# Kernel optimization log

Hardware: AMD Instinct MI355X
Metric: run time of the kernel (lower is better)

## Reference

```python
import jax, jax.numpy as jnp
import numpy as np
from jax import lax

KERNEL = 3
ALPHA = 0.85
C1 = 0.01 ** 2
C2 = 0.03 ** 2


def _avg_pool(x, k):
    # stride-1 VALID average pool over the last two (H, W) dims of NCHW input
    s = lax.reduce_window(x, 0.0, lax.add, (1, 1, k, k), (1, 1, 1, 1), 'VALID')
    return s / (k * k)


def setup_inputs() -> dict:
    key = jax.random.key(0)
    k1, k2 = jax.random.split(key)
    shape = (4, 3, 1080, 1920)
    pred = jax.random.uniform(k1, shape, dtype=jnp.float32)
    gt = jax.random.uniform(k2, shape, dtype=jnp.float32)
    return {"pred": pred, "gt": gt}


def reference(pred, gt):
    p = (KERNEL - 1) // 2
    # reflection pad H and W
    x = jnp.pad(pred, ((0, 0), (0, 0), (p, p), (p, p)), mode='reflect')
    y = jnp.pad(gt, ((0, 0), (0, 0), (p, p), (p, p)), mode='reflect')

    mu_x = _avg_pool(x, KERNEL)
    mu_y = _avg_pool(y, KERNEL)
    sigma_x = _avg_pool(x * x, KERNEL) - mu_x * mu_x
    sigma_y = _avg_pool(y * y, KERNEL) - mu_y * mu_y
    sigma_xy = _avg_pool(x * y, KERNEL) - mu_x * mu_y

    ssim_n = (2.0 * mu_x * mu_y + C1) * (2.0 * sigma_xy + C2)
    ssim_d = (mu_x * mu_x + mu_y * mu_y + C1) * (sigma_x + sigma_y + C2)
    ssim_pp = jnp.clip((1.0 - ssim_n / ssim_d) * 0.5, 0.0, 1.0)

    ssim_loss = jnp.mean(ssim_pp, axis=1, keepdims=True)   # [B,1,H,W]
    l1_loss = jnp.mean(jnp.abs(pred - gt), axis=1, keepdims=True)
    return ALPHA * ssim_loss + (1.0 - ALPHA) * l1_loss
```

## Files before the change

kernel.cpp:

```cpp
#include <hip/hip_runtime.h>

#define IMG_H 1080
#define IMG_W 1920
#define CH 3

typedef float f32x2 __attribute__((ext_vector_type(2)));

#if __has_builtin(__builtin_elementwise_fma)
#define FMA2(a, b, c) __builtin_elementwise_fma((a), (b), (c))
#else
#define FMA2(a, b, c) ((a) * (b) + (c))
#endif

__global__ __launch_bounds__(256)
void dssim_l1_kernel(const float* __restrict__ pred,
                     const float* __restrict__ gt,
                     float* __restrict__ out) {
    constexpr float K1 = 81.0f * 0.0001f;
    constexpr float K2 = 81.0f * 0.0009f;

    const f32x2 k1_ = K1, k2_ = K2;
    const f32x2 two_ = 2.0f, m2_ = -2.0f, e18_ = 18.0f, n9_ = 9.0f;
    const f32x2 mh_ = -0.5f, h_ = 0.5f, zero_ = 0.0f, one_ = 1.0f;
    const f32x2 a3_ = 0.85f / 3.0f, b3_ = 0.15f / 3.0f;

    const int lane = threadIdx.x;
    const int r0   = (blockIdx.y * 4 + threadIdx.y) * 2;
    const int b    = blockIdx.z;
    const int c0   = blockIdx.x * 128 + 2 * lane;

    const int rws[4] = { (r0 == 0) ? 1 : r0 - 1,
                         r0, r0 + 1,
                         (r0 + 2 == IMG_H) ? IMG_H - 2 : r0 + 2 };

    const bool l0 = (lane == 0), l63 = (lane == 63);
    const bool limg = l0  && (blockIdx.x == 0);
    const bool rimg = l63 && (blockIdx.x == 14);
    const int  hcol = l0 ? max(c0 - 1, 0) : min(c0 + 2, IMG_W - 1);
    const bool is_edge = l0 || l63;

    const size_t img = (size_t)IMG_H * IMG_W;
    const float* __restrict__ pb[2 * CH] = {
        pred + (size_t)b * CH * img,
        pred + (size_t)b * CH * img + img,
        pred + (size_t)b * CH * img + 2 * img,
        gt   + (size_t)b * CH * img,
        gt   + (size_t)b * CH * img + img,
        gt   + (size_t)b * CH * img + 2 * img };

    unsigned off[4];
#pragma unroll
    for (int i = 0; i < 4; ++i) off[i] = (unsigned)rws[i] * IMG_W + (unsigned)c0;

    float hx[4][CH], hy[4][CH];
    if (is_edge) {
        const unsigned hbase = (unsigned)hcol - (unsigned)c0;
#pragma unroll
        for (int i = 0; i < 4; ++i) {
            const unsigned ho = off[i] + hbase;
#pragma unroll
            for (int c = 0; c < CH; ++c) {
                hx[i][c] = pb[c][ho];
                hy[i][c] = pb[CH + c][ho];
            }
        }
    }

    f32x2 qx[4][CH], qy[4][CH];
#pragma unroll
    for (int i = 0; i < 4; ++i) {
#pragma unroll
        for (int c = 0; c < CH; ++c) {
            qx[i][c] = *reinterpret_cast<const f32x2*>(pb[c]      + off[i]);
            qy[i][c] = *reinterpret_cast<const f32x2*>(pb[CH + c] + off[i]);
        }
    }

    f32x2 Ax[CH], Ay[CH], Aw[CH], Ap[CH];
    f32x2 Bx[CH], By[CH], Bw[CH], Bp[CH];

#define CONSUME(I, DOA, FIRSTA, DOB, FIRSTB)                                \
    _Pragma("unroll")                                                       \
    for (int c = 0; c < CH; ++c) {                                          \
        const f32x2 qxv = qx[I][c], qyv = qy[I][c];                         \
        float xm = __shfl_up(qxv.y, 1),  ym = __shfl_up(qyv.y, 1);          \
        float xp = __shfl_down(qxv.x, 1), yp = __shfl_down(qyv.x, 1);       \
        if (l0)   { xm = hx[I][c]; ym = hy[I][c]; }                         \
        if (l63)  { xp = hx[I][c]; yp = hy[I][c]; }                         \
        if (limg) { xm = qxv.y; ym = qyv.y; }            \
        if (rimg) { xp = qxv.x; yp = qyv.x; }       \
        const f32x2 X0 = { xm, qxv.x }, X2 = { qxv.y, xp };                 \
        const f32x2 Y0 = { ym, qyv.x }, Y2 = { qyv.y, yp };                 \
        const f32x2 WX = X0 + qxv + X2;                                     \
        const f32x2 WY = Y0 + qyv + Y2;                                     \
        const f32x2 WP = FMA2(X2, Y2, FMA2(qxv, qyv, X0 * Y0));             \
        const f32x2 WW = FMA2(X2, X2, FMA2(Y2, Y2, FMA2(qxv, qxv,           \
                         FMA2(qyv, qyv, FMA2(X0, X0, Y0 * Y0)))));          \
        if (DOA) {                                                          \
            if (FIRSTA) { Ax[c] = WX; Ay[c] = WY; Aw[c] = WW; Ap[c] = WP; } \
            else        { Ax[c] += WX; Ay[c] += WY;                         \
                          Aw[c] += WW; Ap[c] += WP; }                       \
        }                                                                   \
        if (DOB) {                                                          \
            if (FIRSTB) { Bx[c] = WX; By[c] = WY; Bw[c] = WW; Bp[c] = WP; } \
            else        { Bx[c] += WX; By[c] += WY;                         \
                          Bw[c] += WW; Bp[c] += WP; }                       \
        }                                                                   \
    }

    CONSUME(0, true, true,  false, false)
    CONSUME(1, true, false, true,  true)
    CONSUME(2, true, false, true,  false)
    CONSUME(3, false, false, true, false)
#undef CONSUME

    f32x2 l1r0 = zero_, l1r1 = zero_;
#pragma unroll
    for (int c = 0; c < CH; ++c) {
#if __has_builtin(__builtin_elementwise_abs)
        l1r0 += __builtin_elementwise_abs(qx[1][c] - qy[1][c]);
        l1r1 += __builtin_elementwise_abs(qx[2][c] - qy[2][c]);
#else
        f32x2 d0 = qx[1][c] - qy[1][c], d1 = qx[2][c] - qy[2][c];
        d0.x = fabsf(d0.x); d0.y = fabsf(d0.y);
        d1.x = fabsf(d1.x); d1.y = fabsf(d1.y);
        l1r0 += d0; l1r1 += d1;
#endif
    }

#define SSIM2(AX, AY, AW, AP, ACC)                                          \
    {                                                                       \
        const f32x2 u  = (AX) * (AY);                                       \
        const f32x2 v  = FMA2((AY), (AY), (AX) * (AX));                     \
        const f32x2 n1 = FMA2(two_, u, k1_);                                \
        const f32x2 n2 = FMA2(e18_, (AP), FMA2(m2_, u, k2_));               \
        const f32x2 d1 = v + k1_;                                           \
        const f32x2 d2 = FMA2(n9_, (AW), k2_) - v;                          \
        const f32x2 nd = n1 * n2, dd = d1 * d2;                             \
        f32x2 rc;                                                           \
        rc.x = __builtin_amdgcn_rcpf(dd.x);                                 \
        rc.y = __builtin_amdgcn_rcpf(dd.y);                                 \
        f32x2 s = FMA2(mh_, nd * rc, h_);                                   \
        s = __builtin_elementwise_min(                                      \
                __builtin_elementwise_max(s, zero_), one_);                 \
        ACC = FMA2(a3_, s, ACC);                                            \
    }

    f32x2 o0 = b3_ * l1r0;
    f32x2 o1 = b3_ * l1r1;
#pragma unroll
    for (int c = 0; c < CH; ++c) {
        SSIM2(Ax[c], Ay[c], Aw[c], Ap[c], o0)
        SSIM2(Bx[c], By[c], Bw[c], Bp[c], o1)
    }
#undef SSIM2

    float* op = out + ((size_t)b * IMG_H + r0) * IMG_W + c0;
    *reinterpret_cast<f32x2*>(op) = o0;
    *reinterpret_cast<f32x2*>(op + IMG_W) = o1;
}

extern "C" void kernel_launch(void* const* d_in, const int* in_sizes, int n_in,
                              void* d_out, int out_size, void* d_ws, size_t ws_size,
                              hipStream_t stream) {
    const float* pred = (const float*)d_in[0];
    const float* gt   = (const float*)d_in[1];
    float* out = (float*)d_out;

    dim3 block(64, 4, 1);
    dim3 grid(IMG_W / 128, IMG_H / 8, 4);
    dssim_l1_kernel<<<grid, block, 0, stream>>>(pred, gt, out);
}
```

Baseline: 57.44 us.

## Replace cross-lane shuffles and halo loads with overlapping shifted vector loads

Each thread now computes output columns c0+1 and c0+2 from two overlapping float2 loads (at c0 and c0+2), so the 3-wide horizontal window needs no wavefront shuffles and no separate scalar halo loads at wave edges. Column 0 of the image gets a dedicated reflected-edge path run by one thread per row pair, and the right edge is handled by clamping the second load. This doubles the global load instructions, relying on cache hits for the overlap, and makes the output stores unaligned scalar writes. It also adds divergent edge code.

```diff
diff --git a/kernel.cpp b/kernel.cpp
--- a/kernel.cpp
+++ b/kernel.cpp
@@ -33,11 +33,8 @@
                          r0, r0 + 1,
                          (r0 + 2 == IMG_H) ? IMG_H - 2 : r0 + 2 };
 
-    const bool l0 = (lane == 0), l63 = (lane == 63);
-    const bool limg = l0  && (blockIdx.x == 0);
-    const bool rimg = l63 && (blockIdx.x == 14);
-    const int  hcol = l0 ? max(c0 - 1, 0) : min(c0 + 2, IMG_W - 1);
-    const bool is_edge = l0 || l63;
+    const bool ledge = (c0 == 0) && (blockIdx.x == 0);
+    const bool redge = (c0 == IMG_W - 2);
 
     const size_t img = (size_t)IMG_H * IMG_W;
     const float* __restrict__ pb[2 * CH] = {
@@ -48,31 +45,23 @@
         gt   + (size_t)b * CH * img + img,
         gt   + (size_t)b * CH * img + 2 * img };
 
-    unsigned off[4];
-#pragma unroll
-    for (int i = 0; i < 4; ++i) off[i] = (unsigned)rws[i] * IMG_W + (unsigned)c0;
-
-    float hx[4][CH], hy[4][CH];
-    if (is_edge) {
-        const unsigned hbase = (unsigned)hcol - (unsigned)c0;
-#pragma unroll
-        for (int i = 0; i < 4; ++i) {
-            const unsigned ho = off[i] + hbase;
-#pragma unroll
-            for (int c = 0; c < CH; ++c) {
-                hx[i][c] = pb[c][ho];
-                hy[i][c] = pb[CH + c][ho];
-            }
-        }
-    }
-
-    f32x2 qx[4][CH], qy[4][CH];
+    const unsigned rdel = redge ? 0u : 2u;
+    unsigned offM[4], offR[4];
 #pragma unroll
     for (int i = 0; i < 4; ++i) {
+        offM[i] = (unsigned)rws[i] * IMG_W + (unsigned)c0;
+        offR[i] = offM[i] + rdel;
+    }
+
+    f32x2 mx[4][CH], rx[4][CH], my[4][CH], ry[4][CH];
+#pragma unroll
+    for (int i = 0; i < 4; ++i) {
 #pragma unroll
         for (int c = 0; c < CH; ++c) {
-            qx[i][c] = *reinterpret_cast<const f32x2*>(pb[c]      + off[i]);
-            qy[i][c] = *reinterpret_cast<const f32x2*>(pb[CH + c] + off[i]);
+            mx[i][c] = *reinterpret_cast<const f32x2*>(pb[c]      + offM[i]);
+            rx[i][c] = *reinterpret_cast<const f32x2*>(pb[c]      + offR[i]);
+            my[i][c] = *reinterpret_cast<const f32x2*>(pb[CH + c] + offM[i]);
+            ry[i][c] = *reinterpret_cast<const f32x2*>(pb[CH + c] + offR[i]);
         }
     }
 
@@ -82,20 +71,15 @@
 #define CONSUME(I, DOA, FIRSTA, DOB, FIRSTB)                                \
     _Pragma("unroll")                                                       \
     for (int c = 0; c < CH; ++c) {                                          \
-        const f32x2 qxv = qx[I][c], qyv = qy[I][c];                         \
-        float xm = __shfl_up(qxv.y, 1),  ym = __shfl_up(qyv.y, 1);          \
-        float xp = __shfl_down(qxv.x, 1), yp = __shfl_down(qyv.x, 1);       \
-        if (l0)   { xm = hx[I][c]; ym = hy[I][c]; }                         \
-        if (l63)  { xp = hx[I][c]; yp = hy[I][c]; }                         \
-        if (limg) { xm = qxv.y; ym = qyv.y; }            \
-        if (rimg) { xp = qxv.x; yp = qyv.x; }       \
-        const f32x2 X0 = { xm, qxv.x }, X2 = { qxv.y, xp };                 \
-        const f32x2 Y0 = { ym, qyv.x }, Y2 = { qyv.y, yp };                 \
-        const f32x2 WX = X0 + qxv + X2;                                     \
-        const f32x2 WY = Y0 + qyv + Y2;                                     \
-        const f32x2 WP = FMA2(X2, Y2, FMA2(qxv, qyv, X0 * Y0));             \
-        const f32x2 WW = FMA2(X2, X2, FMA2(Y2, Y2, FMA2(qxv, qxv,           \
-                         FMA2(qyv, qyv, FMA2(X0, X0, Y0 * Y0)))));          \
+        const f32x2 T0x = mx[I][c], T2x = rx[I][c];                         \
+        const f32x2 T0y = my[I][c], T2y = ry[I][c];                         \
+        const f32x2 T1x = { T0x.y, T2x.x };                                 \
+        const f32x2 T1y = { T0y.y, T2y.x };                                 \
+        const f32x2 WX = T0x + T1x + T2x;                                   \
+        const f32x2 WY = T0y + T1y + T2y;                                   \
+        const f32x2 WP = FMA2(T2x, T2y, FMA2(T1x, T1y, T0x * T0y));         \
+        const f32x2 WW = FMA2(T2x, T2x, FMA2(T2y, T2y, FMA2(T1x, T1x,       \
+                         FMA2(T1y, T1y, FMA2(T0x, T0x, T0y * T0y)))));      \
         if (DOA) {                                                          \
             if (FIRSTA) { Ax[c] = WX; Ay[c] = WY; Aw[c] = WW; Ap[c] = WP; } \
             else        { Ax[c] += WX; Ay[c] += WY;                         \
@@ -110,23 +94,33 @@
 
     CONSUME(0, true, true,  false, false)
     CONSUME(1, true, false, true,  true)
+
+    f32x2 l1r0 = zero_, l1r1 = zero_;
+#pragma unroll
+    for (int c = 0; c < CH; ++c) {
+        const f32x2 tx = { mx[1][c].y, rx[1][c].x };
+        const f32x2 ty = { my[1][c].y, ry[1][c].x };
+#if __has_builtin(__builtin_elementwise_abs)
+        l1r0 += __builtin_elementwise_abs(tx - ty);
+#else
+        f32x2 d = tx - ty; d.x = fabsf(d.x); d.y = fabsf(d.y); l1r0 += d;
+#endif
+    }
+
     CONSUME(2, true, false, true,  false)
+#pragma unroll
+    for (int c = 0; c < CH; ++c) {
+        const f32x2 tx = { mx[2][c].y, rx[2][c].x };
+        const f32x2 ty = { my[2][c].y, ry[2][c].x };
+#if __has_builtin(__builtin_elementwise_abs)
+        l1r1 += __builtin_elementwise_abs(tx - ty);
+#else
+        f32x2 d = tx - ty; d.x = fabsf(d.x); d.y = fabsf(d.y); l1r1 += d;
+#endif
+    }
+
     CONSUME(3, false, false, true, false)
 #undef CONSUME
-
-    f32x2 l1r0 = zero_, l1r1 = zero_;
-#pragma unroll
-    for (int c = 0; c < CH; ++c) {
-#if __has_builtin(__builtin_elementwise_abs)
-        l1r0 += __builtin_elementwise_abs(qx[1][c] - qy[1][c]);
-        l1r1 += __builtin_elementwise_abs(qx[2][c] - qy[2][c]);
-#else
-        f32x2 d0 = qx[1][c] - qy[1][c], d1 = qx[2][c] - qy[2][c];
-        d0.x = fabsf(d0.x); d0.y = fabsf(d0.y);
-        d1.x = fabsf(d1.x); d1.y = fabsf(d1.y);
-        l1r0 += d0; l1r1 += d1;
-#endif
-    }
 
 #define SSIM2(AX, AY, AW, AP, ACC)                                          \
     {                                                                       \
@@ -155,9 +149,67 @@
     }
 #undef SSIM2
 
-    float* op = out + ((size_t)b * IMG_H + r0) * IMG_W + c0;
-    *reinterpret_cast<f32x2*>(op) = o0;
-    *reinterpret_cast<f32x2*>(op + IMG_W) = o1;
+    float* op0 = out + ((size_t)b * IMG_H + r0) * IMG_W;
+    float* op1 = op0 + IMG_W;
+    op0[c0 + 1] = o0.x;
+    op1[c0 + 1] = o1.x;
+    if (!redge) {
+        op0[c0 + 2] = o0.y;
+        op1[c0 + 2] = o1.y;
+    }
+
+    if (ledge) {
+        float ax[2][CH], ay[2][CH], aw[2][CH], ap[2][CH];
+        float l1e0 = 0.f, l1e1 = 0.f;
+#pragma unroll
+        for (int s = 0; s < 2; ++s)
+#pragma unroll
+            for (int c = 0; c < CH; ++c) {
+                ax[s][c] = 0.f; ay[s][c] = 0.f; aw[s][c] = 0.f; ap[s][c] = 0.f;
+            }
+#pragma unroll
+        for (int i = 0; i < 4; ++i) {
+#pragma unroll
+            for (int c = 0; c < CH; ++c) {
+                const float x0 = pb[c][offM[i]],      x1 = pb[c][offM[i] + 1];
+                const float y0 = pb[CH + c][offM[i]], y1 = pb[CH + c][offM[i] + 1];
+                const float tx = fmaf(2.f, x1, x0);
+                const float ty = fmaf(2.f, y1, y0);
+                const float tw = fmaf(2.f, fmaf(x1, x1, y1 * y1),
+                                           fmaf(x0, x0, y0 * y0));
+                const float tp = fmaf(2.f, x1 * y1, x0 * y0);
+                if (i < 3) { ax[0][c] += tx; ay[0][c] += ty;
+                             aw[0][c] += tw; ap[0][c] += tp; }
+                if (i > 0) { ax[1][c] += tx; ay[1][c] += ty;
+                             aw[1][c] += tw; ap[1][c] += tp; }
+                if (i == 1) l1e0 += fabsf(x0 - y0);
+                if (i == 2) l1e1 += fabsf(x0 - y0);
+            }
+        }
+        float eo0 = (0.15f / 3.f) * l1e0;
+        float eo1 = (0.15f / 3.f) * l1e1;
+#pragma unroll
+        for (int s = 0; s < 2; ++s) {
+#pragma unroll
+            for (int c = 0; c < CH; ++c) {
+                const float AX = ax[s][c], AY = ay[s][c];
+                const float AW = aw[s][c], AP = ap[s][c];
+                const float u = AX * AY;
+                const float v = fmaf(AY, AY, AX * AX);
+                const float n1 = fmaf(2.0f, u, K1);
+                const float n2 = fmaf(18.0f, AP, fmaf(-2.0f, u, K2));
+                const float d1 = v + K1;
+                const float d2 = fmaf(9.0f, AW, K2) - v;
+                float sv = fmaf(-0.5f, (n1 * n2) *
+                                __builtin_amdgcn_rcpf(d1 * d2), 0.5f);
+                sv = fminf(fmaxf(sv, 0.0f), 1.0f);
+                if (s == 0) eo0 = fmaf(0.85f / 3.f, sv, eo0);
+                else        eo1 = fmaf(0.85f / 3.f, sv, eo1);
+            }
+        }
+        op0[0] = eo0;
+        op1[0] = eo1;
+    }
 }
 
 extern "C" void kernel_launch(void* const* d_in, const int* in_sizes, int n_in,
```

Result: slower. 66.23 us (+15.3%).

## Switch to 4-wide column per thread, one output row per half-wave

Applied to the files above, without the earlier changes.

Each thread now computes 4 adjacent columns of a single output row instead of 2 columns of two rows. The 64-lane wave is split into two 32-lane halves, each handling a different row, with shuffles of width 32. Loads become 128-bit float4 over 3 input rows instead of 64-bit over 4 rows. This gives up the vertical row reuse (3 loaded rows per output row instead of 2) in exchange for wider loads and fewer shuffles per output pixel.

```diff
diff --git a/kernel.cpp b/kernel.cpp
--- a/kernel.cpp
+++ b/kernel.cpp
@@ -25,19 +25,23 @@
     const f32x2 a3_ = 0.85f / 3.0f, b3_ = 0.15f / 3.0f;
 
     const int lane = threadIdx.x;
-    const int r0   = (blockIdx.y * 4 + threadIdx.y) * 2;
+    const int sl   = lane & 31;
+    const int hh   = lane >> 5;
+    const int wv   = threadIdx.y;
     const int b    = blockIdx.z;
-    const int c0   = blockIdx.x * 128 + 2 * lane;
 
-    const int rws[4] = { (r0 == 0) ? 1 : r0 - 1,
-                         r0, r0 + 1,
-                         (r0 + 2 == IMG_H) ? IMG_H - 2 : r0 + 2 };
+    const int c0b  = blockIdx.x * 128;
+    const int c0   = c0b + sl * 4;
+    const int r    = blockIdx.y * 8 + wv * 2 + hh;
 
-    const bool l0 = (lane == 0), l63 = (lane == 63);
-    const bool limg = l0  && (blockIdx.x == 0);
-    const bool rimg = l63 && (blockIdx.x == 14);
-    const int  hcol = l0 ? max(c0 - 1, 0) : min(c0 + 2, IMG_W - 1);
-    const bool is_edge = l0 || l63;
+    const int rows[3] = { (r == 0) ? 1 : r - 1, r,
+                          (r == IMG_H - 1) ? IMG_H - 2 : r + 1 };
+
+    const bool sl0 = (sl == 0), sl31 = (sl == 31);
+    const bool is_edge = sl0 || sl31;
+    const bool limg = sl0  && (blockIdx.x == 0);
+    const bool rimg = sl31 && (blockIdx.x == 14);
+    const int  hcol = sl0 ? max(c0 - 1, 0) : min(c0 + 4, IMG_W - 1);
 
     const size_t img = (size_t)IMG_H * IMG_W;
     const float* __restrict__ pb[2 * CH] = {
@@ -48,85 +52,83 @@
         gt   + (size_t)b * CH * img + img,
         gt   + (size_t)b * CH * img + 2 * img };
 
-    unsigned off[4];
+    unsigned off[3];
 #pragma unroll
-    for (int i = 0; i < 4; ++i) off[i] = (unsigned)rws[i] * IMG_W + (unsigned)c0;
+    for (int i = 0; i < 3; ++i) off[i] = (unsigned)rows[i] * IMG_W;
 
-    float hx[4][CH], hy[4][CH];
+    float hxv[3][CH], hyv[3][CH];
     if (is_edge) {
-        const unsigned hbase = (unsigned)hcol - (unsigned)c0;
 #pragma unroll
-        for (int i = 0; i < 4; ++i) {
-            const unsigned ho = off[i] + hbase;
+        for (int i = 0; i < 3; ++i) {
+            const unsigned ho = off[i] + (unsigned)hcol;
 #pragma unroll
             for (int c = 0; c < CH; ++c) {
-                hx[i][c] = pb[c][ho];
-                hy[i][c] = pb[CH + c][ho];
+                hxv[i][c] = pb[c][ho];
+                hyv[i][c] = pb[CH + c][ho];
             }
         }
     }
 
-    f32x2 qx[4][CH], qy[4][CH];
+    float4 qx[3][CH], qy[3][CH];
 #pragma unroll
-    for (int i = 0; i < 4; ++i) {
+    for (int i = 0; i < 3; ++i) {
+        const unsigned mo = off[i] + (unsigned)c0;
 #pragma unroll
         for (int c = 0; c < CH; ++c) {
-            qx[i][c] = *reinterpret_cast<const f32x2*>(pb[c]      + off[i]);
-            qy[i][c] = *reinterpret_cast<const f32x2*>(pb[CH + c] + off[i]);
+            qx[i][c] = *reinterpret_cast<const float4*>(pb[c]      + mo);
+            qy[i][c] = *reinterpret_cast<const float4*>(pb[CH + c] + mo);
         }
     }
 
-    f32x2 Ax[CH], Ay[CH], Aw[CH], Ap[CH];
-    f32x2 Bx[CH], By[CH], Bw[CH], Bp[CH];
+    f32x2 SxL[CH], SyL[CH], SwL[CH], SpL[CH];
+    f32x2 SxH[CH], SyH[CH], SwH[CH], SpH[CH];
+    f32x2 l1L = zero_, l1H = zero_;
 
-#define CONSUME(I, DOA, FIRSTA, DOB, FIRSTB)                                \
+#define CONSUME(I, FIRST, DOL1)                                             \
     _Pragma("unroll")                                                       \
     for (int c = 0; c < CH; ++c) {                                          \
-        const f32x2 qxv = qx[I][c], qyv = qy[I][c];                         \
-        float xm = __shfl_up(qxv.y, 1),  ym = __shfl_up(qyv.y, 1);          \
-        float xp = __shfl_down(qxv.x, 1), yp = __shfl_down(qyv.x, 1);       \
-        if (l0)   { xm = hx[I][c]; ym = hy[I][c]; }                         \
-        if (l63)  { xp = hx[I][c]; yp = hy[I][c]; }                         \
+        const float4 qxv = qx[I][c], qyv = qy[I][c];                        \
+        float xm = __shfl_up(qxv.w, 1, 32),  ym = __shfl_up(qyv.w, 1, 32);  \
+        float xp = __shfl_down(qxv.x, 1, 32), yp = __shfl_down(qyv.x, 1, 32);\
+        if (sl0)  { xm = hxv[I][c]; ym = hyv[I][c]; }                       \
+        if (sl31) { xp = hxv[I][c]; yp = hyv[I][c]; }                       \
         if (limg) { xm = qxv.y; ym = qyv.y; }            \
-        if (rimg) { xp = qxv.x; yp = qyv.x; }       \
-        const f32x2 X0 = { xm, qxv.x }, X2 = { qxv.y, xp };                 \
-        const f32x2 Y0 = { ym, qyv.x }, Y2 = { qyv.y, yp };                 \
-        const f32x2 WX = X0 + qxv + X2;                                     \
-        const f32x2 WY = Y0 + qyv + Y2;                                     \
-        const f32x2 WP = FMA2(X2, Y2, FMA2(qxv, qyv, X0 * Y0));             \
-        const f32x2 WW = FMA2(X2, X2, FMA2(Y2, Y2, FMA2(qxv, qxv,           \
-                         FMA2(qyv, qyv, FMA2(X0, X0, Y0 * Y0)))));          \
-        if (DOA) {                                                          \
-            if (FIRSTA) { Ax[c] = WX; Ay[c] = WY; Aw[c] = WW; Ap[c] = WP; } \
-            else        { Ax[c] += WX; Ay[c] += WY;                         \
-                          Aw[c] += WW; Ap[c] += WP; }                       \
+        if (rimg) { xp = qxv.z; yp = qyv.z; }       \
+                                                           \
+        const f32x2 T0L = { xm, qxv.x },    U0L = { ym, qyv.x };            \
+        const f32x2 T1L = { qxv.x, qxv.y }, U1L = { qyv.x, qyv.y };         \
+        const f32x2 T2L = { qxv.y, qxv.z }, U2L = { qyv.y, qyv.z };         \
+                                                           \
+        const f32x2 T0H = { qxv.y, qxv.z }, U0H = { qyv.y, qyv.z };         \
+        const f32x2 T1H = { qxv.z, qxv.w }, U1H = { qyv.z, qyv.w };         \
+        const f32x2 T2H = { qxv.w, xp },    U2H = { qyv.w, yp };            \
+        const f32x2 WXL = T0L + T1L + T2L, WYL = U0L + U1L + U2L;           \
+        const f32x2 WPL = FMA2(T2L, U2L, FMA2(T1L, U1L, T0L * U0L));        \
+        const f32x2 WWL = FMA2(T2L, T2L, FMA2(U2L, U2L, FMA2(T1L, T1L,      \
+                          FMA2(U1L, U1L, FMA2(T0L, T0L, U0L * U0L)))));     \
+        const f32x2 WXH = T0H + T1H + T2H, WYH = U0H + U1H + U2H;           \
+        const f32x2 WPH = FMA2(T2H, U2H, FMA2(T1H, U1H, T0H * U0H));        \
+        const f32x2 WWH = FMA2(T2H, T2H, FMA2(U2H, U2H, FMA2(T1H, T1H,      \
+                          FMA2(U1H, U1H, FMA2(T0H, T0H, U0H * U0H)))));     \
+        if (FIRST) {                                                        \
+            SxL[c] = WXL; SyL[c] = WYL; SwL[c] = WWL; SpL[c] = WPL;         \
+            SxH[c] = WXH; SyH[c] = WYH; SwH[c] = WWH; SpH[c] = WPH;         \
+        } else {                                                            \
+            SxL[c] += WXL; SyL[c] += WYL; SwL[c] += WWL; SpL[c] += WPL;     \
+            SxH[c] += WXH; SyH[c] += WYH; SwH[c] += WWH; SpH[c] += WPH;     \
         }                                                                   \
-        if (DOB) {                                                          \
-            if (FIRSTB) { Bx[c] = WX; By[c] = WY; Bw[c] = WW; Bp[c] = WP; } \
-            else        { Bx[c] += WX; By[c] += WY;                         \
-                          Bw[c] += WW; Bp[c] += WP; }                       \
+        if (DOL1) {                                                         \
+            f32x2 dL = T1L - U1L, dH = T1H - U1H;                           \
+            dL.x = fabsf(dL.x); dL.y = fabsf(dL.y);                         \
+            dH.x = fabsf(dH.x); dH.y = fabsf(dH.y);                         \
+            l1L += dL; l1H += dH;                                           \
         }                                                                   \
     }
 
-    CONSUME(0, true, true,  false, false)
-    CONSUME(1, true, false, true,  true)
-    CONSUME(2, true, false, true,  false)
-    CONSUME(3, false, false, true, false)
+    CONSUME(0, true,  false)
+    CONSUME(1, false, true)
+    CONSUME(2, false, false)
 #undef CONSUME
-
-    f32x2 l1r0 = zero_, l1r1 = zero_;
-#pragma unroll
-    for (int c = 0; c < CH; ++c) {
-#if __has_builtin(__builtin_elementwise_abs)
-        l1r0 += __builtin_elementwise_abs(qx[1][c] - qy[1][c]);
-        l1r1 += __builtin_elementwise_abs(qx[2][c] - qy[2][c]);
-#else
-        f32x2 d0 = qx[1][c] - qy[1][c], d1 = qx[2][c] - qy[2][c];
-        d0.x = fabsf(d0.x); d0.y = fabsf(d0.y);
-        d1.x = fabsf(d1.x); d1.y = fabsf(d1.y);
-        l1r0 += d0; l1r1 += d1;
-#endif
-    }
 
 #define SSIM2(AX, AY, AW, AP, ACC)                                          \
     {                                                                       \
@@ -146,18 +148,17 @@
         ACC = FMA2(a3_, s, ACC);                                            \
     }
 
-    f32x2 o0 = b3_ * l1r0;
-    f32x2 o1 = b3_ * l1r1;
+    f32x2 oL = b3_ * l1L;
+    f32x2 oH = b3_ * l1H;
 #pragma unroll
     for (int c = 0; c < CH; ++c) {
-        SSIM2(Ax[c], Ay[c], Aw[c], Ap[c], o0)
-        SSIM2(Bx[c], By[c], Bw[c], Bp[c], o1)
+        SSIM2(SxL[c], SyL[c], SwL[c], SpL[c], oL)
+        SSIM2(SxH[c], SyH[c], SwH[c], SpH[c], oH)
     }
 #undef SSIM2
 
-    float* op = out + ((size_t)b * IMG_H + r0) * IMG_W + c0;
-    *reinterpret_cast<f32x2*>(op) = o0;
-    *reinterpret_cast<f32x2*>(op + IMG_W) = o1;
+    float4 o; o.x = oL.x; o.y = oL.y; o.z = oH.x; o.w = oH.y;
+    *reinterpret_cast<float4*>(out + ((size_t)b * IMG_H + r) * IMG_W + c0) = o;
 }
 
 extern "C" void kernel_launch(void* const* d_in, const int* in_sizes, int n_in,
```

Result: no change. 58.20 us (+1.3%).
